# Performance work log

Hardware: AMD Instinct MI355X
Metric: run time of the kernel (lower is better)

The kernel has to match this reference:

```python
import jax, jax.numpy as jnp
import numpy as np

B, N, DIM = 16, 784, 512
H, KD, VD = 8, 64, 256  # num_heads, key_dim, val_dim (attn_ratio=4)
RES = 28
EPS = 1e-5
SCALE = KD ** -0.5


def _make_bias_idxs():
    # pos: [2, N] grid coordinates; rel_pos[0]*RES + rel_pos[1]
    yy, xx = np.meshgrid(np.arange(RES), np.arange(RES), indexing='ij')
    pos = np.stack([yy.reshape(-1), xx.reshape(-1)])  # [2, N]
    rel = np.abs(pos[:, :, None] - pos[:, None, :])   # [2, N, N]
    return jnp.asarray(rel[0] * RES + rel[1], dtype=jnp.int32)


def _bn(x, gamma, beta, mean, var):
    return (x - mean) * (gamma * jax.lax.rsqrt(var + EPS)) + beta


def setup_inputs() -> dict:
    key = jax.random.key(0)
    ks = jax.random.split(key, 12)
    qkv_out = (2 * KD + VD) * H  # 3072
    return {
        'x': jax.random.normal(ks[0], (B, N, DIM), jnp.float32),
        'qkv_w': jax.random.normal(ks[1], (qkv_out, DIM), jnp.float32) * (DIM ** -0.5),
        'qkv_gamma': jax.random.uniform(ks[2], (qkv_out,), jnp.float32, 0.5, 1.5),
        'qkv_beta': jax.random.normal(ks[3], (qkv_out,), jnp.float32) * 0.1,
        'qkv_mean': jax.random.normal(ks[4], (qkv_out,), jnp.float32) * 0.1,
        'qkv_var': jax.random.uniform(ks[5], (qkv_out,), jnp.float32, 0.5, 1.5),
        'attention_biases': jax.random.normal(ks[6], (H, RES * RES), jnp.float32) * 0.02,
        'proj_w': jax.random.normal(ks[7], (DIM, VD * H), jnp.float32) * ((VD * H) ** -0.5),
        'proj_gamma': jax.random.uniform(ks[8], (DIM,), jnp.float32, 0.5, 1.5),
        'proj_beta': jax.random.normal(ks[9], (DIM,), jnp.float32) * 0.1,
        'proj_mean': jax.random.normal(ks[10], (DIM,), jnp.float32) * 0.1,
        'proj_var': jax.random.uniform(ks[11], (DIM,), jnp.float32, 0.5, 1.5),
        'bias_idxs': _make_bias_idxs(),
    }


def reference(x, qkv_w, qkv_gamma, qkv_beta, qkv_mean, qkv_var,
              attention_biases, proj_w, proj_gamma, proj_beta,
              proj_mean, proj_var, bias_idxs):
    # QKV: Linear (no bias) + BatchNorm1d (eval/fused form)
    qkv = _bn(jnp.einsum('bnc,oc->bno', x, qkv_w),
              qkv_gamma, qkv_beta, qkv_mean, qkv_var)        # [B, N, 3072]
    qkv = qkv.reshape(B, N, H, 2 * KD + VD)
    q = qkv[..., :KD].transpose(0, 2, 1, 3)                  # [B, H, N, KD]
    k = qkv[..., KD:2 * KD].transpose(0, 2, 1, 3)            # [B, H, N, KD]
    v = qkv[..., 2 * KD:].transpose(0, 2, 1, 3)              # [B, H, N, VD]

    bias = attention_biases[:, bias_idxs]                    # [H, N, N]
    attn = jnp.einsum('bhnd,bhmd->bhnm', q, k) * SCALE + bias
    attn = jax.nn.softmax(attn, axis=-1)
    out = jnp.einsum('bhnm,bhmd->bhnd', attn, v)             # [B, H, N, VD]
    out = out.transpose(0, 2, 1, 3).reshape(B, N, H * VD)    # [B, N, 2048]

    # proj: SiLU -> Linear (no bias) -> BN (eval/fused form)
    out = jax.nn.silu(out)
    out = _bn(jnp.einsum('bnv,cv->bnc', out, proj_w),
              proj_gamma, proj_beta, proj_mean, proj_var)    # [B, N, DIM]
    return out
```

## Files before the change

kernel.cpp:

```cpp
#include <hip/hip_runtime.h>

#define Bsz 16
#define Nseq 784
#define DIM 512
#define NH 8
#define KD 64
#define VD 256
#define QKV_OUT 3072
#define HV 2048
#define NN 614656

typedef __attribute__((ext_vector_type(8))) short short8;
typedef __attribute__((ext_vector_type(4))) float floatx4;

#define OSTR 136

#if __has_builtin(__builtin_amdgcn_exp2f)
#define EXP2(x) __builtin_amdgcn_exp2f(x)
#else
#define EXP2(x) exp2f(x)
#endif

__device__ __forceinline__ unsigned short f2bf(float f) {
  union { float f; unsigned u; } v; v.f = f;
  unsigned r = v.u + 0x7fffu + ((v.u >> 16) & 1u);
  return (unsigned short)(r >> 16);
}
__device__ __forceinline__ float bf2f(unsigned short u) {
  union { unsigned u; float f; } v; v.u = ((unsigned)u) << 16;
  return v.f;
}

__device__ __forceinline__ void glds16(const unsigned short* g, unsigned short* l) {
  __builtin_amdgcn_global_load_lds(
      (const __attribute__((address_space(1))) void*)g,
      (__attribute__((address_space(3))) void*)l, 16, 0, 0);
}

#define N4X 1605632
#define N4Q 393216
#define N4P 262144
__global__ void cvt_all_kernel(const float* __restrict__ x,
                               const float* __restrict__ qw,
                               const float* __restrict__ pw,
                               unsigned short* __restrict__ xb,
                               unsigned short* __restrict__ wq,
                               unsigned short* __restrict__ wp) {
  int i = blockIdx.x * 256 + threadIdx.x;
  const float4* s; ushort4* d; int off;
  if (i < N4X)              { s = (const float4*)x;  d = (ushort4*)xb; off = i; }
  else if (i < N4X + N4Q)   { s = (const float4*)qw; d = (ushort4*)wq; off = i - N4X; }
  else if (i < N4X + N4Q + N4P) { s = (const float4*)pw; d = (ushort4*)wp; off = i - N4X - N4Q; }
  else return;
  float4 v = s[off];
  ushort4 o;
  o.x = f2bf(v.x); o.y = f2bf(v.y); o.z = f2bf(v.z); o.w = f2bf(v.w);
  d[off] = o;
}

__global__ void bias_pre_kernel(const float* __restrict__ biases,
                                const int* __restrict__ bias_idxs,
                                unsigned short* __restrict__ bias_tab) {
  int t = blockIdx.x * 256 + threadIdx.x;
  if (t >= NN) return;
  int idx = bias_idxs[t];
  for (int h = 0; h < NH; ++h)
    bias_tab[(size_t)h * NN + t] = f2bf(biases[h * Nseq + idx]);
}

__global__ __launch_bounds__(256, 2) void qkv_gemm_kernel(
    const unsigned short* __restrict__ A,
    const unsigned short* __restrict__ Bw,
    const float* __restrict__ gamma, const float* __restrict__ beta,
    const float* __restrict__ mean,  const float* __restrict__ var,
    unsigned short* __restrict__ qo,
    unsigned short* __restrict__ ko,
    unsigned short* __restrict__ vto)
{
  const int K = DIM;
  __shared__ unsigned short smem[128 * OSTR];
  int tid = threadIdx.x;
  int wave = tid >> 6, lane = tid & 63;
  int quad = lane >> 4, l16 = lane & 15;
  int wm = wave >> 1, wn = wave & 1;
  int m0 = blockIdx.y * 128, n0 = blockIdx.x * 128;

  int srow = wave * 32 + (lane >> 2);
  int sch = (lane & 3) * 8;
  const unsigned short* Ab = A + (size_t)(m0 + srow) * K + sch;
  const unsigned short* Bb = Bw + (size_t)(n0 + srow) * K + sch;
  unsigned short* AsW = &smem[wave * 1024];
  unsigned short* BsW = &smem[4096 + wave * 1024];

  floatx4 acc[4][4];
  for (int i = 0; i < 4; ++i)
    for (int j = 0; j < 4; ++j) acc[i][j] = (floatx4)0.0f;

  glds16(Ab, AsW);
  glds16(Ab + 16 * K, AsW + 512);
  glds16(Bb, BsW);
  glds16(Bb + 16 * K, BsW + 512);

  for (int k = 0; k < 16; ++k) {
    int cur = k & 1, nb = cur ^ 1;
    __builtin_amdgcn_s_waitcnt(0xC07F);
    __builtin_amdgcn_s_barrier();
    int k0n = ((k + 1) & 15) * 32;
    glds16(Ab + k0n, AsW + nb * 8192);
    glds16(Ab + k0n + 16 * K, AsW + nb * 8192 + 512);
    glds16(Bb + k0n, BsW + nb * 8192);
    glds16(Bb + k0n + 16 * K, BsW + nb * 8192 + 512);
    __builtin_amdgcn_s_waitcnt(0x0F74);
    __builtin_amdgcn_s_barrier();

    const unsigned short* As = &smem[cur * 8192];
    const unsigned short* Bs = &smem[4096 + cur * 8192];
    short8 af[4], bfr[4];
    for (int mt = 0; mt < 4; ++mt)
      af[mt] = *(const short8*)&As[(wm * 64 + mt * 16 + l16) * 32 + quad * 8];
    for (int nt = 0; nt < 4; ++nt)
      bfr[nt] = *(const short8*)&Bs[(wn * 64 + nt * 16 + l16) * 32 + quad * 8];
    for (int mt = 0; mt < 4; ++mt)
      for (int nt = 0; nt < 4; ++nt)
        acc[mt][nt] = __builtin_amdgcn_mfma_f32_16x16x32_bf16(af[mt], bfr[nt], acc[mt][nt], 0, 0, 0);
  }

  int tt = n0 % 384;
  int h = n0 / 384;
  __builtin_amdgcn_s_waitcnt(0x0070);
  __syncthreads();

  if (tt == 0) {
    for (int nt = 0; nt < 4; ++nt) {
      int o = n0 + wn * 64 + nt * 16 + l16;
      float sc = gamma[o] * rsqrtf(var[o] + 1e-5f);
      float bb = beta[o] - mean[o] * sc;
      if (wn == 0) { sc *= 0.125f; bb *= 0.125f; }
      int jl = wn * 64 + nt * 16 + l16;
      for (int mt = 0; mt < 4; ++mt)
        for (int r = 0; r < 4; ++r) {
          int ml = wm * 64 + mt * 16 + quad * 4 + r;
          smem[ml * OSTR + jl] = f2bf(acc[mt][nt][r] * sc + bb);
        }
    }
    __syncthreads();
    for (int i = 0; i < 8; ++i) {
      int c = i * 256 + tid;
      int ml = c >> 4, jc = c & 15;
      int m = m0 + ml;
      int b = m / 784, n = m - b * 784;
      uint4 v = *(uint4*)&smem[ml * OSTR + jc * 8];
      int j = jc * 8;
      if (j < 64) *(uint4*)&qo[(((size_t)b * NH + h) * Nseq + n) * KD + j] = v;
      else        *(uint4*)&ko[(((size_t)b * NH + h) * Nseq + n) * KD + (j - 64)] = v;
    }
  } else {
    for (int nt = 0; nt < 4; ++nt) {
      int o = n0 + wn * 64 + nt * 16 + l16;
      float sc = gamma[o] * rsqrtf(var[o] + 1e-5f);
      float bb = beta[o] - mean[o] * sc;
      int cl = wn * 64 + nt * 16 + l16;
      for (int mt = 0; mt < 4; ++mt)
        for (int r = 0; r < 4; ++r) {
          int ml = wm * 64 + mt * 16 + quad * 4 + r;
          smem[cl * OSTR + ml] = f2bf(acc[mt][nt][r] * sc + bb);
        }
    }
    __syncthreads();
    int cbase = tt - 128;
    for (int i = 0; i < 8; ++i) {
      int c = i * 256 + tid;
      int cl = c >> 4, mc = c & 15;
      int m = m0 + mc * 8;
      int b = m / 784, n = m - b * 784;
      uint4 v = *(uint4*)&smem[cl * OSTR + mc * 8];
      *(uint4*)&vto[(((size_t)b * NH + h) * VD + cbase + cl) * Nseq + n] = v;
    }
  }
}

__global__ __launch_bounds__(512, 2) void attn_kernel(
    const unsigned short* __restrict__ qb,
    const unsigned short* __restrict__ kb,
    const unsigned short* __restrict__ vtb,
    const unsigned short* __restrict__ bias_tab,
    unsigned short* __restrict__ U)
{
  __shared__ unsigned short vt_lds[2 * 256 * 64];
  __shared__ unsigned short k_lds[2 * 64 * 64];
  __shared__ unsigned short bs_lds[2 * 128 * 64];
  __shared__ unsigned short ps_lds[8 * 16 * 64];
  int tid = threadIdx.x;
  int wave = tid >> 6, lane = tid & 63;
  int quad = lane >> 4, l16 = lane & 15;

  int L = blockIdx.x;
  int xcd = L & 7;
  int s = L >> 3;
  int qp = s % 7;
  int bg = s / 7;
  int bh = bg * 8 + xcd;
  int b = bg, h = xcd;
  int row_base = qp * 128 + wave * 16;

  const unsigned short* brow = bias_tab + (size_t)h * NN;

  int lc = lane >> 3;
  int lch = (lane & 7) ^ lc;
  int sw = l16 & 7;

  const unsigned short* vsrc[4];
#pragma unroll
  for (int t = 0; t < 4; ++t)
    vsrc[t] = vtb + ((size_t)bh * VD + t * 64 + wave * 8 + lc) * Nseq + lch * 8;
  const unsigned short* ksrc =
      kb + (size_t)bh * (Nseq * KD) + (wave * 8 + lc) * KD + lch * 8;
  const unsigned short* bsrc[2];
#pragma unroll
  for (int t = 0; t < 2; ++t) {
    int ig = qp * 128 + t * 64 + wave * 8 + lc;
    if (ig > Nseq - 1) ig = Nseq - 1;
    bsrc[t] = brow + (size_t)ig * Nseq + lch * 8;
  }

  short8 qf[2];
  {
    int qrow = row_base + l16;
    const unsigned short* qp_ = qb + ((size_t)bh * Nseq + qrow) * KD;
    qf[0] = *(const short8*)(qp_ + quad * 8);
    qf[1] = *(const short8*)(qp_ + 32 + quad * 8);
  }

#pragma unroll
  for (int t = 0; t < 4; ++t)
    glds16(vsrc[t], &vt_lds[(t * 64 + wave * 8) * 64]);
  glds16(ksrc, &k_lds[wave * 512]);
#pragma unroll
  for (int t = 0; t < 2; ++t)
    glds16(bsrc[t], &bs_lds[(t * 64 + wave * 8) * 64]);

  float lsum = 0.0f;
  floatx4 oacc[16];
#pragma unroll
  for (int ct = 0; ct < 16; ++ct) oacc[ct] = (floatx4)0.0f;

  unsigned short* psW = &ps_lds[wave * 1024];

  for (int kt = 0; kt < 13; ++kt) {
    int cur = kt & 1;
    int nb = cur ^ 1;
    __builtin_amdgcn_s_waitcnt(0xC07F);
    __builtin_amdgcn_s_barrier();

    int ktn = kt + 1; if (ktn >= 13) ktn = 0;
#pragma unroll
    for (int t = 0; t < 4; ++t)
      glds16(vsrc[t] + ktn * 64, &vt_lds[nb * 16384 + (t * 64 + wave * 8) * 64]);
    glds16(ksrc + (size_t)ktn * 4096, &k_lds[nb * 4096 + wave * 512]);
#pragma unroll
    for (int t = 0; t < 2; ++t)
      glds16(bsrc[t] + ktn * 64, &bs_lds[nb * 8192 + (t * 64 + wave * 8) * 64]);

    __builtin_amdgcn_s_waitcnt(0x0F77);
    __builtin_amdgcn_s_barrier();

    const unsigned short* kbuf = &k_lds[cur * 4096];
    const unsigned short* vbuf = &vt_lds[cur * 16384];
    const unsigned short* bbuf = &bs_lds[cur * 8192];

    floatx4 st[4];
#pragma unroll
    for (int jt = 0; jt < 4; ++jt) {
      int row = jt * 16 + l16;
      short8 kf0 = *(const short8*)&kbuf[row * 64 + (quad ^ sw) * 8];
      short8 kf1 = *(const short8*)&kbuf[row * 64 + ((quad + 4) ^ sw) * 8];
      st[jt] = (floatx4)0.0f;
      st[jt] = __builtin_amdgcn_mfma_f32_16x16x32_bf16(kf0, qf[0], st[jt], 0, 0, 0);
      st[jt] = __builtin_amdgcn_mfma_f32_16x16x32_bf16(kf1, qf[1], st[jt], 0, 0, 0);
    }

    bool tail = (kt == 12);
#pragma unroll
    for (int jt = 0; jt < 4; ++jt) {
      int ch = ((jt << 1) + (quad >> 1)) ^ sw;
      int half = (quad & 1) * 4;
      ushort4 bv = *(const ushort4*)&bbuf[(wave * 16 + l16) * 64 + ch * 8 + half];
      float p0 = EXP2((st[jt][0] + bf2f(bv.x)) * 1.44269504f);
      float p1 = EXP2((st[jt][1] + bf2f(bv.y)) * 1.44269504f);
      float p2 = EXP2((st[jt][2] + bf2f(bv.z)) * 1.44269504f);
      float p3 = EXP2((st[jt][3] + bf2f(bv.w)) * 1.44269504f);
      if (tail && jt > 0) { p0 = 0.0f; p1 = 0.0f; p2 = 0.0f; p3 = 0.0f; }
      lsum += (p0 + p1) + (p2 + p3);
      unsigned lo = (unsigned)f2bf(p0) | ((unsigned)f2bf(p1) << 16);
      unsigned hi = (unsigned)f2bf(p2) | ((unsigned)f2bf(p3) << 16);
      *(uint2*)&psW[l16 * 64 + ch * 8 + half] = make_uint2(lo, hi);
    }

#pragma unroll
    for (int ks = 0; ks < 2; ++ks) {
      short8 pf = *(const short8*)&psW[l16 * 64 + ((ks * 4 + quad) ^ sw) * 8];
#pragma unroll
      for (int ct = 0; ct < 16; ++ct) {
        int c = ct * 16 + l16;
        short8 vf = *(const short8*)&vbuf[c * 64 + ((ks * 4 + quad) ^ sw) * 8];
        oacc[ct] = __builtin_amdgcn_mfma_f32_16x16x32_bf16(pf, vf, oacc[ct], 0, 0, 0);
      }
    }
  }

  __builtin_amdgcn_s_waitcnt(0x0070);

  float tot = lsum;
  tot += __shfl_xor(tot, 16);
  tot += __shfl_xor(tot, 32);
  float inv[4];
#pragma unroll
  for (int r = 0; r < 4; ++r) {
    float lr = __shfl(tot, (lane & 48) | (quad * 4 + r));
    inv[r] = 1.0f / lr;
  }
#pragma unroll
  for (int r = 0; r < 4; ++r) {
    int ig = row_base + quad * 4 + r;
    if (ig >= Nseq) continue;
    size_t base = ((size_t)b * Nseq + ig) * HV + h * VD;
#pragma unroll
    for (int ct = 0; ct < 16; ++ct) {
      float u = oacc[ct][r] * inv[r];
      float sg = 1.0f / (1.0f + EXP2(-u * 1.44269504f));
      U[base + ct * 16 + l16] = f2bf(u * sg);
    }
  }
}

__global__ __launch_bounds__(256, 2) void proj_gemm_kernel(
    const unsigned short* __restrict__ Ubuf,
    const unsigned short* __restrict__ Wp,
    const float* __restrict__ gamma, const float* __restrict__ beta,
    const float* __restrict__ mean,  const float* __restrict__ var,
    float* __restrict__ out)
{
  const int K = HV;
  __shared__ unsigned short smem[16384];
  int tid = threadIdx.x;
  int wave = tid >> 6, lane = tid & 63;
  int quad = lane >> 4, l16 = lane & 15;
  int wm = wave >> 1, wn = wave & 1;
  int o0 = blockIdx.y * 128, mB = blockIdx.x * 128;

  int srow = wave * 32 + (lane >> 2);
  int sch = (lane & 3) * 8;
  const unsigned short* Ab = Wp + (size_t)(o0 + srow) * K + sch;
  const unsigned short* Bb = Ubuf + (size_t)(mB + srow) * K + sch;
  unsigned short* AsW = &smem[wave * 1024];
  unsigned short* BsW = &smem[4096 + wave * 1024];

  floatx4 acc[4][4];
  for (int i = 0; i < 4; ++i)
    for (int j = 0; j < 4; ++j) acc[i][j] = (floatx4)0.0f;

  glds16(Ab, AsW);
  glds16(Ab + 16 * K, AsW + 512);
  glds16(Bb, BsW);
  glds16(Bb + 16 * K, BsW + 512);

  for (int k = 0; k < 64; ++k) {
    int cur = k & 1, nb = cur ^ 1;
    __builtin_amdgcn_s_waitcnt(0xC07F);
    __builtin_amdgcn_s_barrier();
    int k0n = ((k + 1) & 63) * 32;
    glds16(Ab + k0n, AsW + nb * 8192);
    glds16(Ab + k0n + 16 * K, AsW + nb * 8192 + 512);
    glds16(Bb + k0n, BsW + nb * 8192);
    glds16(Bb + k0n + 16 * K, BsW + nb * 8192 + 512);
    __builtin_amdgcn_s_waitcnt(0x0F74);
    __builtin_amdgcn_s_barrier();

    const unsigned short* As = &smem[cur * 8192];
    const unsigned short* Bs = &smem[4096 + cur * 8192];
    short8 af[4], bfr[4];
    for (int mt = 0; mt < 4; ++mt)
      af[mt] = *(const short8*)&As[(wm * 64 + mt * 16 + l16) * 32 + quad * 8];
    for (int nt = 0; nt < 4; ++nt)
      bfr[nt] = *(const short8*)&Bs[(wn * 64 + nt * 16 + l16) * 32 + quad * 8];
    for (int mt = 0; mt < 4; ++mt)
      for (int nt = 0; nt < 4; ++nt)
        acc[mt][nt] = __builtin_amdgcn_mfma_f32_16x16x32_bf16(af[mt], bfr[nt], acc[mt][nt], 0, 0, 0);
  }
  __builtin_amdgcn_s_waitcnt(0x0070);

  for (int mt = 0; mt < 4; ++mt) {
    int ob = o0 + wm * 64 + mt * 16 + quad * 4;
    float4 g = *(const float4*)&gamma[ob];
    float4 vr = *(const float4*)&var[ob];
    float4 mn = *(const float4*)&mean[ob];
    float4 bt = *(const float4*)&beta[ob];
    float sc0 = g.x * rsqrtf(vr.x + 1e-5f), bb0 = bt.x - mn.x * sc0;
    float sc1 = g.y * rsqrtf(vr.y + 1e-5f), bb1 = bt.y - mn.y * sc1;
    float sc2 = g.z * rsqrtf(vr.z + 1e-5f), bb2 = bt.z - mn.z * sc2;
    float sc3 = g.w * rsqrtf(vr.w + 1e-5f), bb3 = bt.w - mn.w * sc3;
    for (int nt = 0; nt < 4; ++nt) {
      int m = mB + wn * 64 + nt * 16 + l16;
      float4 v;
      v.x = acc[mt][nt][0] * sc0 + bb0;
      v.y = acc[mt][nt][1] * sc1 + bb1;
      v.z = acc[mt][nt][2] * sc2 + bb2;
      v.w = acc[mt][nt][3] * sc3 + bb3;
      *(float4*)&out[(size_t)m * DIM + ob] = v;
    }
  }
}

extern "C" void kernel_launch(void* const* d_in, const int* in_sizes, int n_in,
                              void* d_out, int out_size, void* d_ws, size_t ws_size,
                              hipStream_t stream) {
  const float* x          = (const float*)d_in[0];
  const float* qkv_w      = (const float*)d_in[1];
  const float* qkv_gamma  = (const float*)d_in[2];
  const float* qkv_beta   = (const float*)d_in[3];
  const float* qkv_mean   = (const float*)d_in[4];
  const float* qkv_var    = (const float*)d_in[5];
  const float* att_biases = (const float*)d_in[6];
  const float* proj_w     = (const float*)d_in[7];
  const float* proj_gamma = (const float*)d_in[8];
  const float* proj_beta  = (const float*)d_in[9];
  const float* proj_mean  = (const float*)d_in[10];
  const float* proj_var   = (const float*)d_in[11];
  const int*   bias_idxs  = (const int*)d_in[12];
  float* out = (float*)d_out;

  char* ws = (char*)d_ws;
  unsigned short* xb  = (unsigned short*)(ws);
  unsigned short* bias_tab = (unsigned short*)(ws);
  unsigned short* wq  = (unsigned short*)(ws + 12845056);
  unsigned short* wp  = (unsigned short*)(ws + 15990784);
  unsigned short* qo  = (unsigned short*)(ws + 18087936);
  unsigned short* ko  = (unsigned short*)(ws + 30932992);
  unsigned short* vto = (unsigned short*)(ws + 43778048);
  unsigned short* Ub  = (unsigned short*)(ws + 95158272);

  {
    int n4 = N4X + N4Q + N4P;
    cvt_all_kernel<<<(n4 + 255) / 256, 256, 0, stream>>>(x, qkv_w, proj_w, xb, wq, wp);
  }

  qkv_gemm_kernel<<<dim3(QKV_OUT / 128, (Bsz * Nseq) / 128), 256, 0, stream>>>(
      xb, wq, qkv_gamma, qkv_beta, qkv_mean, qkv_var, qo, ko, vto);

  bias_pre_kernel<<<(NN + 255) / 256, 256, 0, stream>>>(att_biases, bias_idxs, bias_tab);

  attn_kernel<<<7 * Bsz * NH, 512, 0, stream>>>(qo, ko, vto, bias_tab, Ub);

  proj_gemm_kernel<<<dim3((Bsz * Nseq) / 128, DIM / 128), 256, 0, stream>>>(
      Ub, wp, proj_gamma, proj_beta, proj_mean, proj_var, out);
}
```

Baseline: 337.8 us.

## Retile attention kernel with 32x32 MFMA and shared P tile across waves

Each wave used to own 16 query rows and run the full PV product over all 256 value columns with 16x16x32 MFMAs. Now the block's 128x64 score tile is split over the 8 waves with 32x32x16 MFMAs, and the P tile is written to shared LDS. The PV product is then split as a 2x4 grid of 64x64 output tiles per wave, which cuts repeated V-fragment LDS reads and accumulator register pressure. The cost is an extra block barrier per iteration and a cross-wave row-sum reduction through LDS before the normalize-and-SiLU epilogue.

```diff
diff --git a/kernel.cpp b/kernel.cpp
--- a/kernel.cpp
+++ b/kernel.cpp
@@ -12,8 +12,10 @@
 
 typedef __attribute__((ext_vector_type(8))) short short8;
 typedef __attribute__((ext_vector_type(4))) float floatx4;
+typedef __attribute__((ext_vector_type(16))) float floatx16;
 
 #define OSTR 136
+#define LOG2E 1.44269504f
 
 #if __has_builtin(__builtin_amdgcn_exp2f)
 #define EXP2(x) __builtin_amdgcn_exp2f(x)
@@ -186,13 +188,18 @@
     const unsigned short* __restrict__ bias_tab,
     unsigned short* __restrict__ U)
 {
-  __shared__ unsigned short vt_lds[2 * 256 * 64];
-  __shared__ unsigned short k_lds[2 * 64 * 64];
-  __shared__ unsigned short bs_lds[2 * 128 * 64];
-  __shared__ unsigned short ps_lds[8 * 16 * 64];
+  __shared__ unsigned short smem[65536];
+  unsigned short* vt_lds = smem;
+  unsigned short* k_lds  = smem + 32768;
+  unsigned short* bs_lds = smem + 40960;
+  unsigned short* ps_lds = smem + 57344;
+  float* lsum_lds = (float*)(smem + 32768);
+
   int tid = threadIdx.x;
   int wave = tid >> 6, lane = tid & 63;
-  int quad = lane >> 4, l16 = lane & 15;
+  int l5 = lane >> 5;
+  int i32 = lane & 31;
+  int l7 = lane & 7;
 
   int L = blockIdx.x;
   int xcd = L & 7;
@@ -201,13 +208,17 @@
   int bg = s / 7;
   int bh = bg * 8 + xcd;
   int b = bg, h = xcd;
-  int row_base = qp * 128 + wave * 16;
+
+  int jt = wave >> 2;
+  int it = wave & 3;
+  int rg = wave >> 2;
+  int cg = wave & 3;
+  int iRow = it * 32 + i32;
 
   const unsigned short* brow = bias_tab + (size_t)h * NN;
 
   int lc = lane >> 3;
   int lch = (lane & 7) ^ lc;
-  int sw = l16 & 7;
 
   const unsigned short* vsrc[4];
 #pragma unroll
@@ -223,14 +234,6 @@
     bsrc[t] = brow + (size_t)ig * Nseq + lch * 8;
   }
 
-  short8 qf[2];
-  {
-    int qrow = row_base + l16;
-    const unsigned short* qp_ = qb + ((size_t)bh * Nseq + qrow) * KD;
-    qf[0] = *(const short8*)(qp_ + quad * 8);
-    qf[1] = *(const short8*)(qp_ + 32 + quad * 8);
-  }
-
 #pragma unroll
   for (int t = 0; t < 4; ++t)
     glds16(vsrc[t], &vt_lds[(t * 64 + wave * 8) * 64]);
@@ -239,12 +242,20 @@
   for (int t = 0; t < 2; ++t)
     glds16(bsrc[t], &bs_lds[(t * 64 + wave * 8) * 64]);
 
+  short8 qf[4];
+  {
+    const unsigned short* qpp = qb + ((size_t)bh * Nseq + qp * 128 + iRow) * KD;
+#pragma unroll
+    for (int ks = 0; ks < 4; ++ks)
+      qf[ks] = *(const short8*)(qpp + ks * 16 + l5 * 8);
+  }
+
   float lsum = 0.0f;
-  floatx4 oacc[16];
-#pragma unroll
-  for (int ct = 0; ct < 16; ++ct) oacc[ct] = (floatx4)0.0f;
-
-  unsigned short* psW = &ps_lds[wave * 1024];
+  floatx16 oacc[2][2];
+#pragma unroll
+  for (int rt = 0; rt < 2; ++rt)
+#pragma unroll
+    for (int ct = 0; ct < 2; ++ct) oacc[rt][ct] = (floatx16)0.0f;
 
   for (int kt = 0; kt < 13; ++kt) {
     int cur = kt & 1;
@@ -268,67 +279,73 @@
     const unsigned short* vbuf = &vt_lds[cur * 16384];
     const unsigned short* bbuf = &bs_lds[cur * 8192];
 
-    floatx4 st[4];
-#pragma unroll
-    for (int jt = 0; jt < 4; ++jt) {
-      int row = jt * 16 + l16;
-      short8 kf0 = *(const short8*)&kbuf[row * 64 + (quad ^ sw) * 8];
-      short8 kf1 = *(const short8*)&kbuf[row * 64 + ((quad + 4) ^ sw) * 8];
-      st[jt] = (floatx4)0.0f;
-      st[jt] = __builtin_amdgcn_mfma_f32_16x16x32_bf16(kf0, qf[0], st[jt], 0, 0, 0);
-      st[jt] = __builtin_amdgcn_mfma_f32_16x16x32_bf16(kf1, qf[1], st[jt], 0, 0, 0);
+    floatx16 st = (floatx16)0.0f;
+#pragma unroll
+    for (int ks = 0; ks < 4; ++ks) {
+      short8 kf = *(const short8*)&kbuf[(jt * 32 + i32) * 64 + (((ks << 1) + l5) ^ l7) * 8];
+      st = __builtin_amdgcn_mfma_f32_32x32x16_bf16(kf, qf[ks], st, 0, 0, 0);
     }
 
     bool tail = (kt == 12);
 #pragma unroll
-    for (int jt = 0; jt < 4; ++jt) {
-      int ch = ((jt << 1) + (quad >> 1)) ^ sw;
-      int half = (quad & 1) * 4;
-      ushort4 bv = *(const ushort4*)&bbuf[(wave * 16 + l16) * 64 + ch * 8 + half];
-      float p0 = EXP2((st[jt][0] + bf2f(bv.x)) * 1.44269504f);
-      float p1 = EXP2((st[jt][1] + bf2f(bv.y)) * 1.44269504f);
-      float p2 = EXP2((st[jt][2] + bf2f(bv.z)) * 1.44269504f);
-      float p3 = EXP2((st[jt][3] + bf2f(bv.w)) * 1.44269504f);
-      if (tail && jt > 0) { p0 = 0.0f; p1 = 0.0f; p2 = 0.0f; p3 = 0.0f; }
+    for (int q = 0; q < 4; ++q) {
+      int chunk = ((jt << 2) + q) ^ l7;
+      int off = iRow * 64 + chunk * 8 + l5 * 4;
+      ushort4 bv = *(const ushort4*)&bbuf[off];
+      float p0 = EXP2((st[q * 4 + 0] + bf2f(bv.x)) * LOG2E);
+      float p1 = EXP2((st[q * 4 + 1] + bf2f(bv.y)) * LOG2E);
+      float p2 = EXP2((st[q * 4 + 2] + bf2f(bv.z)) * LOG2E);
+      float p3 = EXP2((st[q * 4 + 3] + bf2f(bv.w)) * LOG2E);
+      if (tail && (jt == 1 || q >= 2)) { p0 = 0.0f; p1 = 0.0f; p2 = 0.0f; p3 = 0.0f; }
       lsum += (p0 + p1) + (p2 + p3);
       unsigned lo = (unsigned)f2bf(p0) | ((unsigned)f2bf(p1) << 16);
       unsigned hi = (unsigned)f2bf(p2) | ((unsigned)f2bf(p3) << 16);
-      *(uint2*)&psW[l16 * 64 + ch * 8 + half] = make_uint2(lo, hi);
-    }
-
-#pragma unroll
-    for (int ks = 0; ks < 2; ++ks) {
-      short8 pf = *(const short8*)&psW[l16 * 64 + ((ks * 4 + quad) ^ sw) * 8];
-#pragma unroll
-      for (int ct = 0; ct < 16; ++ct) {
-        int c = ct * 16 + l16;
-        short8 vf = *(const short8*)&vbuf[c * 64 + ((ks * 4 + quad) ^ sw) * 8];
-        oacc[ct] = __builtin_amdgcn_mfma_f32_16x16x32_bf16(pf, vf, oacc[ct], 0, 0, 0);
+      *(uint2*)&ps_lds[off] = make_uint2(lo, hi);
+    }
+
+    __builtin_amdgcn_s_waitcnt(0xC07F);
+    __builtin_amdgcn_s_barrier();
+
+#pragma unroll
+    for (int ks = 0; ks < 4; ++ks) {
+      int pch = (((ks << 1) + l5) ^ l7) * 8;
+      short8 a0 = *(const short8*)&ps_lds[(rg * 64 + i32) * 64 + pch];
+      short8 a1 = *(const short8*)&ps_lds[(rg * 64 + 32 + i32) * 64 + pch];
+      short8 b0 = *(const short8*)&vbuf[(cg * 64 + i32) * 64 + pch];
+      short8 b1 = *(const short8*)&vbuf[(cg * 64 + 32 + i32) * 64 + pch];
+      oacc[0][0] = __builtin_amdgcn_mfma_f32_32x32x16_bf16(a0, b0, oacc[0][0], 0, 0, 0);
+      oacc[0][1] = __builtin_amdgcn_mfma_f32_32x32x16_bf16(a0, b1, oacc[0][1], 0, 0, 0);
+      oacc[1][0] = __builtin_amdgcn_mfma_f32_32x32x16_bf16(a1, b0, oacc[1][0], 0, 0, 0);
+      oacc[1][1] = __builtin_amdgcn_mfma_f32_32x32x16_bf16(a1, b1, oacc[1][1], 0, 0, 0);
+    }
+  }
+
+  __builtin_amdgcn_s_waitcnt(0x0070);
+  lsum += __shfl_xor(lsum, 32);
+  if (lane < 32) lsum_lds[jt * 128 + iRow] = lsum;
+  __syncthreads();
+  if (tid < 128) {
+    float tot = lsum_lds[tid] + lsum_lds[128 + tid];
+    lsum_lds[tid] = 1.0f / tot;
+  }
+  __syncthreads();
+
+#pragma unroll
+  for (int rt = 0; rt < 2; ++rt) {
+#pragma unroll
+    for (int e = 0; e < 16; ++e) {
+      int row = rg * 64 + rt * 32 + (e & 3) + 8 * (e >> 2) + 4 * l5;
+      int ig = qp * 128 + row;
+      if (ig < Nseq) {
+        float iv = lsum_lds[row];
+        size_t base = ((size_t)b * Nseq + ig) * HV + h * VD + cg * 64;
+        float u0 = oacc[rt][0][e] * iv;
+        float u1 = oacc[rt][1][e] * iv;
+        float s0 = 1.0f / (1.0f + EXP2(-u0 * LOG2E));
+        float s1 = 1.0f / (1.0f + EXP2(-u1 * LOG2E));
+        U[base + i32]      = f2bf(u0 * s0);
+        U[base + 32 + i32] = f2bf(u1 * s1);
       }
-    }
-  }
-
-  __builtin_amdgcn_s_waitcnt(0x0070);
-
-  float tot = lsum;
-  tot += __shfl_xor(tot, 16);
-  tot += __shfl_xor(tot, 32);
-  float inv[4];
-#pragma unroll
-  for (int r = 0; r < 4; ++r) {
-    float lr = __shfl(tot, (lane & 48) | (quad * 4 + r));
-    inv[r] = 1.0f / lr;
-  }
-#pragma unroll
-  for (int r = 0; r < 4; ++r) {
-    int ig = row_base + quad * 4 + r;
-    if (ig >= Nseq) continue;
-    size_t base = ((size_t)b * Nseq + ig) * HV + h * VD;
-#pragma unroll
-    for (int ct = 0; ct < 16; ++ct) {
-      float u = oacc[ct][r] * inv[r];
-      float sg = 1.0f / (1.0f + EXP2(-u * 1.44269504f));
-      U[base + ct * 16 + l16] = f2bf(u * sg);
     }
   }
 }
```

Measured after the change: 341.4 us. No clear change (+1.1%).
